# Optimization experiments

Hardware: AMD Instinct MI355X
Metric: run time of the kernel (lower is better)

Reference implementation:

```python
import jax, jax.numpy as jnp
import numpy as np

D = 256  # feature_dim
NQ = 512
NK = 512


def setup_inputs() -> dict:
    key = jax.random.key(0)
    ks = jax.random.split(key, 12)
    s = 0.05
    return {
        "x": jax.random.normal(ks[0], (1, D, NQ), dtype=jnp.float32),
        "source": jax.random.normal(ks[1], (1, D, NK), dtype=jnp.float32),
        "dist": jax.random.normal(ks[2], (1, D, NQ * NK), dtype=jnp.float32),
        "mask": jax.random.randint(ks[3], (NQ, NK), 0, 2).astype(jnp.bool_),
        # MLPAttention mlp: channels [3D, D, 1] (1x1 convs == per-position matmuls)
        "aW1": jax.random.normal(ks[4], (D, 3 * D), dtype=jnp.float32) * s,
        "ab1": jax.random.normal(ks[5], (D,), dtype=jnp.float32) * s,
        "aW2": jax.random.normal(ks[6], (1, D), dtype=jnp.float32) * s,
        "ab2": jax.random.normal(ks[7], (1,), dtype=jnp.float32) * s,
        # merge mlp: channels [2D, 2D, D], last bias initialized to 0
        "mW1": jax.random.normal(ks[8], (2 * D, 2 * D), dtype=jnp.float32) * s,
        "mb1": jax.random.normal(ks[9], (2 * D,), dtype=jnp.float32) * s,
        "mW2": jax.random.normal(ks[10], (D, 2 * D), dtype=jnp.float32) * s,
        "mb2": jnp.zeros((D,), dtype=jnp.float32),
    }


def _conv1x1(W, b, x):
    # Conv1d(kernel_size=1): (out,in) @ (b,in,n) -> (b,out,n)
    return jnp.einsum('oc,bcn->bon', W, x) + b[None, :, None]


def reference(x, source, dist, mask, aW1, ab1, aW2, ab2, mW1, mb1, mW2, mb2):
    nq, nk = x.shape[-1], source.shape[-1]
    d = x.shape[1]
    # broadcast query over keys and key over queries, flatten to (1, d, nq*nk)
    qb = jnp.broadcast_to(x[:, :, :, None], (1, d, nq, nk)).reshape(1, d, nq * nk)
    kb = jnp.broadcast_to(source[:, :, None, :], (1, d, nq, nk)).reshape(1, d, nq * nk)
    feat = jnp.concatenate([qb, kb, dist], axis=1)  # (1, 3d, nq*nk)
    h = jax.nn.relu(_conv1x1(aW1, ab1, feat))       # (1, d, nq*nk)
    scores = _conv1x1(aW2, ab2, h).reshape(1, nq, nk)
    # boolean-mask branch: push masked-out entries far below the min
    neg = jax.lax.stop_gradient(scores.min()) - 20.0
    scores = scores + neg * (~mask).astype(scores.dtype)[None]
    prob = jax.nn.softmax(scores, axis=-1)
    message = jnp.einsum('bnm,bdm->bdn', prob, source)  # value == source
    # merge MLP on concat([x, message])
    cat = jnp.concatenate([x, message], axis=1)  # (1, 2d, nq)
    h2 = jax.nn.relu(_conv1x1(mW1, mb1, cat))
    out = _conv1x1(mW2, mb2, h2)  # (1, d, nq)
    return (out, scores)
```

## Files before the change

kernel.cpp:

```cpp
#include <hip/hip_runtime.h>
#include <stdint.h>

#define D_ 256
#define NQ_ 512
#define NK_ 512
#define NP_ (NQ_*NK_)

typedef __attribute__((ext_vector_type(8))) __bf16 bf16x8;
typedef __attribute__((ext_vector_type(4))) float f32x4;

__device__ __forceinline__ unsigned short f2bf(float f) {
  unsigned u = __builtin_bit_cast(unsigned, f);
  u += 0x7FFFu + ((u >> 16) & 1u);
  return (unsigned short)(u >> 16);
}
__device__ __forceinline__ unsigned encf(float f) {
  unsigned u = __builtin_bit_cast(unsigned, f);
  return (u & 0x80000000u) ? ~u : (u | 0x80000000u);
}
__device__ __forceinline__ float decf(unsigned e) {
  unsigned u = (e & 0x80000000u) ? (e ^ 0x80000000u) : ~e;
  return __builtin_bit_cast(float, u);
}

template<int EPI, int KTILES>
__device__ __forceinline__ void gemm_body(
    const unsigned short* __restrict__ A, int lda,
    const unsigned short* __restrict__ B, int ldb,
    const float* __restrict__ bias,
    void* __restrict__ Dst, int ldd, int nTilesN, int bid) {
  const int t = threadIdx.x, w = t >> 6, l = t & 63, l15 = l & 15, g = l >> 4;
  const int bm = bid / nTilesN, bn = bid % nTilesN;
  const int m0 = bm*64 + w*16, n0 = bn*64;
  const unsigned short* Ap = A + (size_t)(m0 + l15)*lda + g*8;
  const unsigned short* Bp = B + (size_t)(n0 + l15)*ldb + g*8;
  f32x4 acc[4];
  #pragma unroll
  for (int n = 0; n < 4; ++n) acc[n] = (f32x4){0.f,0.f,0.f,0.f};
  #pragma unroll 2
  for (int kk = 0; kk < KTILES; ++kk) {
    bf16x8 a = *(const bf16x8*)(Ap + kk*32);
    #pragma unroll
    for (int n = 0; n < 4; ++n) {
      bf16x8 b = *(const bf16x8*)(Bp + (size_t)n*16*ldb + kk*32);
      acc[n] = __builtin_amdgcn_mfma_f32_16x16x32_bf16(a, b, acc[n], 0, 0, 0);
    }
  }
  #pragma unroll
  for (int n = 0; n < 4; ++n) {
    const int col = n0 + n*16 + l15;
    const float bc = (EPI & 4) ? bias[col] : 0.f;
    #pragma unroll
    for (int r = 0; r < 4; ++r) {
      const int m = m0 + g*4 + r;
      float v = acc[n][r] + bc;
      if (EPI & 8) v += bias[m];
      if (EPI & 2) v = fmaxf(v, 0.f);
      if (EPI & 1) ((unsigned short*)Dst)[(size_t)m*ldd + col] = f2bf(v);
      else         ((float*)Dst)[(size_t)m*ldd + col] = v;
    }
  }
}

template<int EPI, int KTILES>
__global__ __launch_bounds__(256) void gemm_k(
    const unsigned short* __restrict__ A, int lda,
    const unsigned short* __restrict__ B, int ldb,
    const float* __restrict__ bias,
    void* __restrict__ Dst, int ldd, int nTilesN) {
  gemm_body<EPI, KTILES>(A, lda, B, ldb, bias, Dst, ldd, nTilesN, blockIdx.x);
}

__global__ __launch_bounds__(256) void kprep(
    const unsigned* __restrict__ maskw, unsigned* __restrict__ wsMin,
    unsigned* __restrict__ wsFlag,
    const float* __restrict__ aW1, const float* __restrict__ source,
    const float* __restrict__ x, const float* __restrict__ mW1,
    const float* __restrict__ mW2,
    unsigned short* __restrict__ Ab, unsigned short* __restrict__ srcbf,
    unsigned short* __restrict__ mW1b, unsigned short* __restrict__ mW2b,
    unsigned short* __restrict__ aW1A, unsigned short* __restrict__ aW1B,
    unsigned short* __restrict__ catT, unsigned short* __restrict__ srcT) {
  __shared__ float tile[64][65];
  const int b = blockIdx.x, t = threadIdx.x;
  if (b == 0) {
    if (t < 64) {
      unsigned a01 = 1, af = 1;
      for (int i = 0; i < 4; ++i) {
        unsigned v = maskw[t*4 + i];
        a01 &= (v == 0u || v == 1u) ? 1u : 0u;
        af  &= (v == 0u || v == 0x3f800000u) ? 1u : 0u;
      }
      unsigned long long b01 = __ballot(a01 != 0), bf = __ballot(af != 0);
      if (t == 0) {
        *wsFlag = (b01 == ~0ull) ? 1u : ((bf == ~0ull) ? 2u : 0u);
        *wsMin = 0xFFFFFFFFu;
      }
    }
    return;
  }
  if (b < 705) {
    const int bb = b - 1;
    const float* src; unsigned short* dst;
    if (bb < 64) {
      int j = bb*1024 + t*4;
      int img = j >> 9, li = (j >> 3) & 63, i0 = j & 7;
      int row = ((img >> 2) & 3)*64 + (img & 3)*16 + (li & 15);
      int ch  = (img >> 4)*32 + (li >> 4)*8 + i0;
      src = aW1 + row*768 + 512 + ch; dst = Ab + j;
    }
    else if (bb < 192)  { int j = (bb-64)*1024 + t*4;  src = source + j;    dst = srcbf + j; }
    else if (bb < 448)  { int j = (bb-192)*1024 + t*4; src = mW1 + j;       dst = mW1b + j; }
    else if (bb < 576)  { int j = (bb-448)*1024 + t*4; src = mW2 + j;       dst = mW2b + j; }
    else if (bb < 640)  { int j = (bb-576)*1024 + t*4; int e=j>>8, c=j&255; src = aW1 + e*768 + c;       dst = aW1A + j; }
    else                { int j = (bb-640)*1024 + t*4; int e=j>>8, c=j&255; src = aW1 + e*768 + 256 + c; dst = aW1B + j; }
    const float4 v = *(const float4*)src;
    ushort4 o; o.x=f2bf(v.x); o.y=f2bf(v.y); o.z=f2bf(v.z); o.w=f2bf(v.w);
    *(ushort4*)dst = o;
    return;
  }
  const float* src; unsigned short* dst; int ldd, bid;
  if (b < 737) { src = x;      dst = catT; ldd = 512; bid = b - 705; }
  else         { src = source; dst = srcT; ldd = 256; bid = b - 737; }
  const int bd = bid >> 3, bq = bid & 7;
  const int r = t >> 4, c4 = (t & 15) * 4;
  #pragma unroll
  for (int rr = 0; rr < 4; ++rr) {
    int dl = rr*16 + r;
    float4 v = *(const float4*)(src + (size_t)(bd*64 + dl)*512 + bq*64 + c4);
    tile[dl][c4+0] = v.x; tile[dl][c4+1] = v.y; tile[dl][c4+2] = v.z; tile[dl][c4+3] = v.w;
  }
  __syncthreads();
  #pragma unroll
  for (int rr = 0; rr < 4; ++rr) {
    int j = rr*16 + r;
    ushort4 o;
    o.x = f2bf(tile[c4+0][j]); o.y = f2bf(tile[c4+1][j]);
    o.z = f2bf(tile[c4+2][j]); o.w = f2bf(tile[c4+3][j]);
    *(ushort4*)(dst + (size_t)(bq*64 + j)*ldd + bd*64 + c4) = o;
  }
}

__global__ __launch_bounds__(256) void kprep2(
    const unsigned short* __restrict__ catT, const unsigned short* __restrict__ aW1A,
    const float* __restrict__ ab1, float* __restrict__ Up,
    const unsigned short* __restrict__ srcT, const unsigned short* __restrict__ aW1B,
    float* __restrict__ VmT) {
  if (blockIdx.x < 32)
    gemm_body<4, 8>(catT, 512, aW1A, 256, ab1, (void*)Up, 256, 4, blockIdx.x);
  else
    gemm_body<0, 8>(srcT, 256, aW1B, 256, (const float*)nullptr, (void*)VmT, 256, 4, blockIdx.x - 32);
}

__device__ __forceinline__ void loads8(float (&s)[8], const float* __restrict__ dbase,
                                       int kk, int quad1, int quad2) {
  #pragma unroll
  for (int i = 0; i < 4; ++i) s[i]   = dbase[(size_t)(kk*32 + quad1*4 + i) * NP_];
  #pragma unroll
  for (int i = 0; i < 4; ++i) s[4+i] = dbase[(size_t)(kk*32 + quad2*4 + i) * NP_];
}
__device__ __forceinline__ void cvtwrite(unsigned char* __restrict__ buf, const float (&s)[8],
                                         int l, int quad1, int quad2) {
  const int key = (l >> 1) & 3;
  {
    unsigned lo = (unsigned)f2bf(s[0]) | ((unsigned)f2bf(s[1]) << 16);
    unsigned hi = (unsigned)f2bf(s[2]) | ((unsigned)f2bf(s[3]) << 16);
    *(uint2*)(buf + l*64 + ((((quad1>>1) ^ key) << 4) | ((quad1 & 1) << 3))) = make_uint2(lo, hi);
  }
  {
    unsigned lo = (unsigned)f2bf(s[4]) | ((unsigned)f2bf(s[5]) << 16);
    unsigned hi = (unsigned)f2bf(s[6]) | ((unsigned)f2bf(s[7]) << 16);
    *(uint2*)(buf + l*64 + ((((quad2>>1) ^ key) << 4) | ((quad2 & 1) << 3))) = make_uint2(lo, hi);
  }
}
__device__ __forceinline__ void loadA(bf16x8 (&a)[4], const unsigned short* __restrict__ Ab,
                                      int kk, int w, int l) {
  #pragma unroll
  for (int m = 0; m < 4; ++m)
    a[m] = *(const bf16x8*)(Ab + ((kk*16 + w*4 + m) << 9) + l*8);
}
__device__ __forceinline__ void computeStep(f32x4 (&acc)[4][4], const bf16x8 (&a)[4],
                                            const unsigned char* __restrict__ buf,
                                            int l15, int g) {
  bf16x8 bfrag[4];
  #pragma unroll
  for (int n = 0; n < 4; ++n) {
    const int p = n*16 + l15;
    bfrag[n] = *(const bf16x8*)(buf + p*64 + ((g ^ ((p >> 1) & 3)) << 4));
  }
  #pragma unroll
  for (int m = 0; m < 4; ++m)
    #pragma unroll
    for (int n = 0; n < 4; ++n)
      acc[m][n] = __builtin_amdgcn_mfma_f32_16x16x32_bf16(a[m], bfrag[n], acc[m][n], 0, 0, 0);
}

__global__ __launch_bounds__(256, 2) void kscores3(
    const float* __restrict__ dist, const unsigned short* __restrict__ Ab,
    const float* __restrict__ VmT, const float* __restrict__ Up,
    const float* __restrict__ aW2, const float* __restrict__ ab2,
    float* __restrict__ outScores, unsigned* __restrict__ wsMin) {
  __shared__ __align__(16) unsigned char ldsB[2][4096];
  __shared__ float red[4][64];

  const int t = threadIdx.x, w = t >> 6, l = t & 63, l15 = l & 15, g = l >> 4;
  const int bs = (blockIdx.x & 7) * 128 + (blockIdx.x >> 3);
  const int base_tile = bs * 4;

  const int quad1 = (w + g) & 3;
  const int quad2 = quad1 + 4;

  float aw[4][4];
  #pragma unroll
  for (int m = 0; m < 4; ++m) {
    const float4 v = *(const float4*)(aW2 + w*64 + m*16 + g*4);
    aw[m][0]=v.x; aw[m][1]=v.y; aw[m][2]=v.z; aw[m][3]=v.w;
  }
  const float ab2v = ab2[0];

  float s[4][8];
  {
    const float* db0 = dist + (size_t)base_tile*64 + l;
    loads8(s[0], db0, 0, quad1, quad2);
    loads8(s[1], db0, 1, quad1, quad2);
    loads8(s[2], db0, 2, quad1, quad2);
  }

  for (int tt = 0; tt < 4; ++tt) {
    const int p0 = (base_tile + tt) * 64;
    const int q  = p0 >> 9;
    const int k0 = p0 & 511;
    const float* dbase = dist + (size_t)p0 + l;

    f32x4 acc[4][4];
    #pragma unroll
    for (int m = 0; m < 4; ++m) {
      const float4 u = *(const float4*)(Up + q*256 + w*64 + m*16 + g*4);
      #pragma unroll
      for (int n = 0; n < 4; ++n) {
        acc[m][n][0]=u.x; acc[m][n][1]=u.y; acc[m][n][2]=u.z; acc[m][n][3]=u.w;
      }
    }

    bf16x8 af[2][4];
    loadA(af[0], Ab, 0, w, l);

    #pragma unroll
    for (int kk = 0; kk < 8; ++kk) {
      const int bb = kk & 1;
      cvtwrite(ldsB[bb], s[kk & 3], l, quad1, quad2);
      if (kk < 5) {
        loads8(s[(kk + 3) & 3], dbase, kk + 3, quad1, quad2);
      } else if (tt < 3) {
        loads8(s[(kk + 3) & 3], dbase + 64, kk - 5, quad1, quad2);
      }
      __builtin_amdgcn_sched_barrier(0);
      asm volatile("s_waitcnt lgkmcnt(0)" ::: "memory");
      __builtin_amdgcn_s_barrier();
      __builtin_amdgcn_sched_barrier(0);
      if (kk < 7) loadA(af[(kk + 1) & 1], Ab, kk + 1, w, l);
      computeStep(acc, af[kk & 1], ldsB[bb], l15, g);
    }

    float part[4];
    #pragma unroll
    for (int n = 0; n < 4; ++n) {
      const int j = k0 + n*16 + l15;
      float s2 = 0.f;
      #pragma unroll
      for (int m = 0; m < 4; ++m) {
        const float4 v4 = *(const float4*)(VmT + (size_t)j*256 + w*64 + m*16 + g*4);
        s2 += aw[m][0] * fmaxf(acc[m][n][0] + v4.x, 0.f);
        s2 += aw[m][1] * fmaxf(acc[m][n][1] + v4.y, 0.f);
        s2 += aw[m][2] * fmaxf(acc[m][n][2] + v4.z, 0.f);
        s2 += aw[m][3] * fmaxf(acc[m][n][3] + v4.w, 0.f);
      }
      s2 += __shfl_xor(s2, 16);
      s2 += __shfl_xor(s2, 32);
      part[n] = s2;
    }
    __builtin_amdgcn_s_barrier();
    if (l < 16) {
      #pragma unroll
      for (int n = 0; n < 4; ++n) red[w][n*16 + l] = part[n];
    }
    asm volatile("s_waitcnt lgkmcnt(0)" ::: "memory");
    __builtin_amdgcn_s_barrier();
    if (t < 64) {
      float s2 = red[0][t] + red[1][t] + red[2][t] + red[3][t] + ab2v;
      outScores[p0 + t] = s2;
      float mn = s2;
      #pragma unroll
      for (int off = 32; off; off >>= 1) mn = fminf(mn, __shfl_xor(mn, off));
      if (t == 0) atomicMin(wsMin, encf(mn));
    }
  }
}

__global__ __launch_bounds__(256) void ksoftmax(
    const void* __restrict__ maskp,
    const unsigned* __restrict__ wsMin, const unsigned* __restrict__ wsFlag,
    float* __restrict__ scores, unsigned short* __restrict__ prob) {
  __shared__ float srow[512];
  __shared__ float redl[8];
  const int t = threadIdx.x, w = t >> 6, l = t & 63;
  const int q = blockIdx.x;
  const float neg = decf(*wsMin) - 20.0f;
  const unsigned flag = *wsFlag;

  for (int k = t; k < 512; k += 256) {
    float raw = scores[q*512 + k];
    bool mv;
    if (flag == 1)      mv = ((const int*)maskp)[q*512 + k] != 0;
    else if (flag == 2) mv = ((const float*)maskp)[q*512 + k] != 0.f;
    else                mv = ((const unsigned char*)maskp)[q*512 + k] != 0;
    float ms = raw + (mv ? 0.f : neg);
    scores[q*512 + k] = ms;
    srow[k] = ms;
  }
  __syncthreads();
  float lm = fmaxf(srow[t], srow[t + 256]);
  #pragma unroll
  for (int off = 32; off; off >>= 1) lm = fmaxf(lm, __shfl_xor(lm, off));
  if (l == 0) redl[w] = lm;
  __syncthreads();
  float rmax = fmaxf(fmaxf(redl[0], redl[1]), fmaxf(redl[2], redl[3]));
  float e0 = __expf(srow[t] - rmax), e1 = __expf(srow[t + 256] - rmax);
  float ls = e0 + e1;
  #pragma unroll
  for (int off = 32; off; off >>= 1) ls += __shfl_xor(ls, off);
  if (l == 0) redl[4 + w] = ls;
  __syncthreads();
  float inv = 1.0f / (redl[4] + redl[5] + redl[6] + redl[7]);
  prob[q*512 + t]       = f2bf(e0 * inv);
  prob[q*512 + t + 256] = f2bf(e1 * inv);
}

extern "C" void kernel_launch(void* const* d_in, const int* in_sizes, int n_in,
                              void* d_out, int out_size, void* d_ws, size_t ws_size,
                              hipStream_t stream) {
  const float* x      = (const float*)d_in[0];
  const float* source = (const float*)d_in[1];
  const float* dist   = (const float*)d_in[2];
  const void*  mask   = (const void*)d_in[3];
  const float* aW1    = (const float*)d_in[4];
  const float* ab1    = (const float*)d_in[5];
  const float* aW2    = (const float*)d_in[6];
  const float* ab2    = (const float*)d_in[7];
  const float* mW1    = (const float*)d_in[8];
  const float* mb1    = (const float*)d_in[9];
  const float* mW2    = (const float*)d_in[10];
  const float* mb2    = (const float*)d_in[11];

  float* outMain = (float*)d_out;
  float* scores  = outMain + 256*512;

  char* ws = (char*)d_ws;
  unsigned* wsMin  = (unsigned*)ws;
  unsigned* wsFlag = wsMin + 1;
  unsigned short* Ab    = (unsigned short*)(ws + 1024);
  float*          Up    = (float*)(ws + 132096);
  float*          VmT   = (float*)(ws + 656384);
  unsigned short* srcbf = (unsigned short*)(ws + 1180672);
  unsigned short* srcT  = (unsigned short*)(ws + 1442816);
  unsigned short* mW1b  = (unsigned short*)(ws + 1704960);
  unsigned short* mW2b  = (unsigned short*)(ws + 2229248);
  unsigned short* aW1A  = (unsigned short*)(ws + 2491392);
  unsigned short* aW1B  = (unsigned short*)(ws + 2622464);
  unsigned short* catT  = (unsigned short*)(ws + 2753536);
  unsigned short* prob  = (unsigned short*)(ws + 3277824);
  unsigned short* h2T   = (unsigned short*)(ws + 3802112);

  hipLaunchKernelGGL(kprep, dim3(769), dim3(256), 0, stream,
                     (const unsigned*)mask, wsMin, wsFlag, aW1, source, x, mW1, mW2,
                     Ab, srcbf, mW1b, mW2b, aW1A, aW1B, catT, srcT);
  hipLaunchKernelGGL(kprep2, dim3(64), dim3(256), 0, stream,
                     catT, aW1A, ab1, Up, srcT, aW1B, VmT);
  hipLaunchKernelGGL(kscores3, dim3(1024), dim3(256), 0, stream,
                     dist, Ab, VmT, Up, aW2, ab2, scores, wsMin);
  hipLaunchKernelGGL(ksoftmax, dim3(512), dim3(256), 0, stream,
                     mask, wsMin, wsFlag, scores, prob);
  hipLaunchKernelGGL((gemm_k<1, 16>), dim3(32), dim3(256), 0, stream,
                     prob, 512, srcbf, 512, (const float*)nullptr, (void*)(catT + 256), 512, 4);
  hipLaunchKernelGGL((gemm_k<7, 16>), dim3(64), dim3(256), 0, stream,
                     catT, 512, mW1b, 512, mb1, (void*)h2T, 512, 8);
  hipLaunchKernelGGL((gemm_k<8, 16>), dim3(32), dim3(256), 0, stream,
                     mW2b, 512, h2T, 512, mb2, (void*)outMain, 512, 8);
}
```

Baseline: 167.1 us.

## Widen scores kernel tile to 128 positions per step to reuse weight fragments

The scores kernel now handles 128 positions per iteration instead of 64. Each wave computes a 4x8 MFMA accumulator block, so each A-weight fragment load is reused across twice as many columns. The dist prefetch depth drops from three stages to two, and the LDS writes become 16-byte stores. The grid is halved to 512 blocks. In exchange, the 128 accumulator floats per thread raise register pressure under launch_bounds(256,2), and the shallower prefetch gives less room to hide dist loads.

```diff
diff --git a/kernel.cpp b/kernel.cpp
--- a/kernel.cpp
+++ b/kernel.cpp
@@ -13,6 +13,9 @@
   unsigned u = __builtin_bit_cast(unsigned, f);
   u += 0x7FFFu + ((u >> 16) & 1u);
   return (unsigned short)(u >> 16);
+}
+__device__ __forceinline__ unsigned pk2(float a, float b) {
+  return (unsigned)f2bf(a) | ((unsigned)f2bf(b) << 16);
 }
 __device__ __forceinline__ unsigned encf(float f) {
   unsigned u = __builtin_bit_cast(unsigned, f);
@@ -152,25 +155,30 @@
     gemm_body<0, 8>(srcT, 256, aW1B, 256, (const float*)nullptr, (void*)VmT, 256, 4, blockIdx.x - 32);
 }
 
-__device__ __forceinline__ void loads8(float (&s)[8], const float* __restrict__ dbase,
-                                       int kk, int quad1, int quad2) {
-  #pragma unroll
-  for (int i = 0; i < 4; ++i) s[i]   = dbase[(size_t)(kk*32 + quad1*4 + i) * NP_];
-  #pragma unroll
-  for (int i = 0; i < 4; ++i) s[4+i] = dbase[(size_t)(kk*32 + quad2*4 + i) * NP_];
-}
-__device__ __forceinline__ void cvtwrite(unsigned char* __restrict__ buf, const float (&s)[8],
-                                         int l, int quad1, int quad2) {
+__device__ __forceinline__ void loads16(float (&s)[16], const float* __restrict__ dbase,
+                                        int kk, int wq) {
+  #pragma unroll
+  for (int qi = 0; qi < 4; ++qi) {
+    const int quad = wq*2 + (qi & 1) + (qi >> 1)*4;
+    #pragma unroll
+    for (int i = 0; i < 4; ++i)
+      s[qi*4 + i] = dbase[(size_t)(kk*32 + quad*4 + i) * NP_];
+  }
+}
+__device__ __forceinline__ void cvtwrite16(unsigned char* __restrict__ buf, const float (&s)[16],
+                                           int l, int wq) {
   const int key = (l >> 1) & 3;
   {
-    unsigned lo = (unsigned)f2bf(s[0]) | ((unsigned)f2bf(s[1]) << 16);
-    unsigned hi = (unsigned)f2bf(s[2]) | ((unsigned)f2bf(s[3]) << 16);
-    *(uint2*)(buf + l*64 + ((((quad1>>1) ^ key) << 4) | ((quad1 & 1) << 3))) = make_uint2(lo, hi);
+    uint4 o;
+    o.x = pk2(s[0], s[1]);  o.y = pk2(s[2], s[3]);
+    o.z = pk2(s[4], s[5]);  o.w = pk2(s[6], s[7]);
+    *(uint4*)(buf + l*64 + ((wq ^ key) << 4)) = o;
   }
   {
-    unsigned lo = (unsigned)f2bf(s[4]) | ((unsigned)f2bf(s[5]) << 16);
-    unsigned hi = (unsigned)f2bf(s[6]) | ((unsigned)f2bf(s[7]) << 16);
-    *(uint2*)(buf + l*64 + ((((quad2>>1) ^ key) << 4) | ((quad2 & 1) << 3))) = make_uint2(lo, hi);
+    uint4 o;
+    o.x = pk2(s[8],  s[9]);  o.y = pk2(s[10], s[11]);
+    o.z = pk2(s[12], s[13]); o.w = pk2(s[14], s[15]);
+    *(uint4*)(buf + l*64 + (((wq + 2) ^ key) << 4)) = o;
   }
 }
 __device__ __forceinline__ void loadA(bf16x8 (&a)[4], const unsigned short* __restrict__ Ab,
@@ -179,36 +187,19 @@
   for (int m = 0; m < 4; ++m)
     a[m] = *(const bf16x8*)(Ab + ((kk*16 + w*4 + m) << 9) + l*8);
 }
-__device__ __forceinline__ void computeStep(f32x4 (&acc)[4][4], const bf16x8 (&a)[4],
-                                            const unsigned char* __restrict__ buf,
-                                            int l15, int g) {
-  bf16x8 bfrag[4];
-  #pragma unroll
-  for (int n = 0; n < 4; ++n) {
-    const int p = n*16 + l15;
-    bfrag[n] = *(const bf16x8*)(buf + p*64 + ((g ^ ((p >> 1) & 3)) << 4));
-  }
-  #pragma unroll
-  for (int m = 0; m < 4; ++m)
-    #pragma unroll
-    for (int n = 0; n < 4; ++n)
-      acc[m][n] = __builtin_amdgcn_mfma_f32_16x16x32_bf16(a[m], bfrag[n], acc[m][n], 0, 0, 0);
-}
-
-__global__ __launch_bounds__(256, 2) void kscores3(
+
+__global__ __launch_bounds__(256, 2) void kscores3w(
     const float* __restrict__ dist, const unsigned short* __restrict__ Ab,
     const float* __restrict__ VmT, const float* __restrict__ Up,
     const float* __restrict__ aW2, const float* __restrict__ ab2,
     float* __restrict__ outScores, unsigned* __restrict__ wsMin) {
-  __shared__ __align__(16) unsigned char ldsB[2][4096];
-  __shared__ float red[4][64];
+  __shared__ __align__(16) unsigned char ldsB[2][2][4096];
+  __shared__ float red[4][128];
 
   const int t = threadIdx.x, w = t >> 6, l = t & 63, l15 = l & 15, g = l >> 4;
-  const int bs = (blockIdx.x & 7) * 128 + (blockIdx.x >> 3);
-  const int base_tile = bs * 4;
-
-  const int quad1 = (w + g) & 3;
-  const int quad2 = quad1 + 4;
+  const int half = w >> 1, wq = w & 1;
+  const int bs = (blockIdx.x & 7) * 64 + (blockIdx.x >> 3);
+  const int base_pair = bs * 512;
 
   float aw[4][4];
   #pragma unroll
@@ -218,53 +209,58 @@
   }
   const float ab2v = ab2[0];
 
-  float s[4][8];
+  float s[2][16];
   {
-    const float* db0 = dist + (size_t)base_tile*64 + l;
-    loads8(s[0], db0, 0, quad1, quad2);
-    loads8(s[1], db0, 1, quad1, quad2);
-    loads8(s[2], db0, 2, quad1, quad2);
+    const float* db0 = dist + (size_t)base_pair + half*64 + l;
+    loads16(s[0], db0, 0, wq);
+    loads16(s[1], db0, 1, wq);
   }
 
   for (int tt = 0; tt < 4; ++tt) {
-    const int p0 = (base_tile + tt) * 64;
+    const int p0 = base_pair + tt*128;
     const int q  = p0 >> 9;
     const int k0 = p0 & 511;
-    const float* dbase = dist + (size_t)p0 + l;
-
-    f32x4 acc[4][4];
+    const float* dbase = dist + (size_t)p0 + half*64 + l;
+
+    f32x4 acc[4][8];
     #pragma unroll
     for (int m = 0; m < 4; ++m) {
       const float4 u = *(const float4*)(Up + q*256 + w*64 + m*16 + g*4);
       #pragma unroll
-      for (int n = 0; n < 4; ++n) {
+      for (int n = 0; n < 8; ++n) {
         acc[m][n][0]=u.x; acc[m][n][1]=u.y; acc[m][n][2]=u.z; acc[m][n][3]=u.w;
       }
     }
-
-    bf16x8 af[2][4];
-    loadA(af[0], Ab, 0, w, l);
 
     #pragma unroll
     for (int kk = 0; kk < 8; ++kk) {
       const int bb = kk & 1;
-      cvtwrite(ldsB[bb], s[kk & 3], l, quad1, quad2);
-      if (kk < 5) {
-        loads8(s[(kk + 3) & 3], dbase, kk + 3, quad1, quad2);
-      } else if (tt < 3) {
-        loads8(s[(kk + 3) & 3], dbase + 64, kk - 5, quad1, quad2);
-      }
+      cvtwrite16(&ldsB[bb][half][0], s[kk & 1], l, wq);
+      if (kk < 6)      loads16(s[kk & 1], dbase, kk + 2, wq);
+      else if (tt < 3) loads16(s[kk & 1], dbase + 128, kk - 6, wq);
+      bf16x8 af[4];
+      loadA(af, Ab, kk, w, l);
       __builtin_amdgcn_sched_barrier(0);
       asm volatile("s_waitcnt lgkmcnt(0)" ::: "memory");
       __builtin_amdgcn_s_barrier();
       __builtin_amdgcn_sched_barrier(0);
-      if (kk < 7) loadA(af[(kk + 1) & 1], Ab, kk + 1, w, l);
-      computeStep(acc, af[kk & 1], ldsB[bb], l15, g);
-    }
-
-    float part[4];
-    #pragma unroll
-    for (int n = 0; n < 4; ++n) {
+      bf16x8 bfrag[8];
+      #pragma unroll
+      for (int n = 0; n < 8; ++n) {
+        const int pl = (n & 3)*16 + l15;
+        const unsigned char* base = &ldsB[bb][n >> 2][0];
+        bfrag[n] = *(const bf16x8*)(base + pl*64 + ((g ^ ((pl >> 1) & 3)) << 4));
+      }
+      #pragma unroll
+      for (int m = 0; m < 4; ++m)
+        #pragma unroll
+        for (int n = 0; n < 8; ++n)
+          acc[m][n] = __builtin_amdgcn_mfma_f32_16x16x32_bf16(af[m], bfrag[n], acc[m][n], 0, 0, 0);
+    }
+
+    float part[8];
+    #pragma unroll
+    for (int n = 0; n < 8; ++n) {
       const int j = k0 + n*16 + l15;
       float s2 = 0.f;
       #pragma unroll
@@ -282,17 +278,17 @@
     __builtin_amdgcn_s_barrier();
     if (l < 16) {
       #pragma unroll
-      for (int n = 0; n < 4; ++n) red[w][n*16 + l] = part[n];
+      for (int n = 0; n < 8; ++n) red[w][n*16 + l] = part[n];
     }
     asm volatile("s_waitcnt lgkmcnt(0)" ::: "memory");
     __builtin_amdgcn_s_barrier();
-    if (t < 64) {
+    if (t < 128) {
       float s2 = red[0][t] + red[1][t] + red[2][t] + red[3][t] + ab2v;
       outScores[p0 + t] = s2;
       float mn = s2;
       #pragma unroll
       for (int off = 32; off; off >>= 1) mn = fminf(mn, __shfl_xor(mn, off));
-      if (t == 0) atomicMin(wsMin, encf(mn));
+      if (l == 0) atomicMin(wsMin, encf(mn));
     }
   }
 }
@@ -376,7 +372,7 @@
                      Ab, srcbf, mW1b, mW2b, aW1A, aW1B, catT, srcT);
   hipLaunchKernelGGL(kprep2, dim3(64), dim3(256), 0, stream,
                      catT, aW1A, ab1, Up, srcT, aW1B, VmT);
-  hipLaunchKernelGGL(kscores3, dim3(1024), dim3(256), 0, stream,
+  hipLaunchKernelGGL(kscores3w, dim3(512), dim3(256), 0, stream,
                      dist, Ab, VmT, Up, aW2, ab2, scores, wsMin);
   hipLaunchKernelGGL(ksoftmax, dim3(512), dim3(256), 0, stream,
                      mask, wsMin, wsFlag, scores, prob);
```

New measurement: 324.4 us. 1.94x slower.
